# Optimization experiments

Measured on AMD Instinct MI355X. Metric: run time of the kernel, lower is better.

The kernel has to match this reference:

```python
import jax, jax.numpy as jnp
import numpy as np

EPS = 1e-8
TAU = 1.0


def graph_conv(h_in, adj, W, b):
    # h: [N, D_out]
    h = h_in @ W
    nrm = jnp.linalg.norm(h, axis=1, keepdims=True)
    h_norm = h / jnp.maximum(nrm, EPS)  # F.normalize with eps clamp
    # cosine-sim logits + log-adjacency mask -> row softmax
    logits = (h_norm @ h_norm.T) / TAU + jnp.log(adj + EPS)  # [N, N]
    attn = jax.nn.softmax(logits, axis=1)
    return attn @ h + b


def setup_inputs() -> dict:
    key = jax.random.key(0)
    ks = jax.random.split(key, 20)
    N, F, H, C = 4096, 512, 128, 16

    def xavier(k, fan_in, fan_out):
        s = float(np.sqrt(6.0 / (fan_in + fan_out)))
        return jax.random.uniform(k, (fan_in, fan_out), minval=-s, maxval=s, dtype=jnp.float32)

    return {
        "x": jax.random.normal(ks[0], (N, F), dtype=jnp.float32),
        "adj_low": jax.random.uniform(ks[1], (N, N), dtype=jnp.float32),
        "adj_high": jax.random.uniform(ks[2], (N, N), dtype=jnp.float32),
        "adj_mid": jax.random.uniform(ks[3], (N, N), dtype=jnp.float32),
        "w_low0": xavier(ks[4], F, H), "b_low0": jnp.zeros((H,), jnp.float32),
        "w_high0": xavier(ks[5], F, H), "b_high0": jnp.zeros((H,), jnp.float32),
        "w_mid0": xavier(ks[6], F, H), "b_mid0": jnp.zeros((H,), jnp.float32),
        "w_low1": xavier(ks[7], H, C), "b_low1": jnp.zeros((C,), jnp.float32),
        "w_high1": xavier(ks[8], H, C), "b_high1": jnp.zeros((C,), jnp.float32),
        "w_mid1": xavier(ks[9], H, C), "b_mid1": jnp.zeros((C,), jnp.float32),
        "g0": jnp.ones((3,), jnp.float32),
        "g1": jnp.ones((3,), jnp.float32),
    }


def reference(x, adj_low, adj_high, adj_mid,
              w_low0, b_low0, w_high0, b_high0, w_mid0, b_mid0,
              w_low1, b_low1, w_high1, b_high1, w_mid1, b_mid1,
              g0, g1):
    # layer 0 (inner layer: ReLU; dropout p=0 in eval mode -> identity)
    hl = jax.nn.relu(graph_conv(x, adj_low, w_low0, b_low0))
    hh = jax.nn.relu(graph_conv(x, adj_high, w_high0, b_high0))
    hm = jax.nn.relu(graph_conv(x, adj_mid, w_mid0, b_mid0))
    w = jax.nn.softmax(g0)
    h = w[0] * hl + w[1] * hh + w[2] * hm

    # layer 1 (final layer: no activation)
    hl = graph_conv(h, adj_low, w_low1, b_low1)
    hh = graph_conv(h, adj_high, w_high1, b_high1)
    hm = graph_conv(h, adj_mid, w_mid1, b_mid1)
    w = jax.nn.softmax(g1)
    h = w[0] * hl + w[1] * hh + w[2] * hm

    return jax.nn.log_softmax(h, axis=-1)
```

## Files before the change

### kernel.cpp

```cpp
#include <hip/hip_runtime.h>

#define N_NODES 4096
#define F_IN 512
#define H_DIM 128
#define C_DIM 16
#define EPSF 1e-8f
#define LOG2E 1.4426950408889634f
#define SMAX 2.0f
#define NKS0 8
#define KLEN0 (N_NODES / NKS0)
#define NT0 (KLEN0 / 32)
#define NKS1 8

typedef __attribute__((ext_vector_type(8))) short bf16x8;
typedef __attribute__((ext_vector_type(4))) short bf16x4;
typedef __attribute__((ext_vector_type(4))) float f32x4;

__device__ __forceinline__ ushort f2bf(float f){
  union { float f; unsigned u; } v; v.f = f;
  unsigned u = v.u;
  return (ushort)((u + 0x7fffu + ((u >> 16) & 1u)) >> 16);
}
__device__ __forceinline__ float bf2f(ushort h){
  union { unsigned u; float f; } v; v.u = ((unsigned)h) << 16;
  return v.f;
}

__global__ __launch_bounds__(256) void proj0_kernel(
    const float* __restrict__ x,
    const float* __restrict__ Wl, const float* __restrict__ Wh,
    const float* __restrict__ Wm,
    ushort* __restrict__ hn, ushort* __restrict__ hvT)
{
  const int t = threadIdx.x;
  const int d = t & 127;
  const int half = t >> 7;
  const int r0 = blockIdx.x * 8;
  __shared__ float xs[8][F_IN];
  for (int i = t; i < 8 * F_IN; i += 256)
    xs[i >> 9][i & 511] = x[(size_t)(r0 + (i >> 9)) * F_IN + (i & 511)];
  __syncthreads();

  float acc0[8], acc1[8], acc2[8];
#pragma unroll
  for (int r = 0; r < 8; r++) { acc0[r] = 0.f; acc1[r] = 0.f; acc2[r] = 0.f; }

  const int k0 = half * (F_IN / 2);
  for (int k = k0; k < k0 + F_IN / 2; k++) {
    float wl = Wl[k * H_DIM + d];
    float wh = Wh[k * H_DIM + d];
    float wm = Wm[k * H_DIM + d];
#pragma unroll
    for (int r = 0; r < 8; r++) {
      float xv = xs[r][k];
      acc0[r] = fmaf(xv, wl, acc0[r]);
      acc1[r] = fmaf(xv, wh, acc1[r]);
      acc2[r] = fmaf(xv, wm, acc2[r]);
    }
  }

  __shared__ float part[3][8][128];
  if (half == 1) {
#pragma unroll
    for (int r = 0; r < 8; r++) {
      part[0][r][d] = acc0[r]; part[1][r][d] = acc1[r]; part[2][r][d] = acc2[r];
    }
  }
  __syncthreads();
  if (half == 0) {
#pragma unroll
    for (int r = 0; r < 8; r++) {
      acc0[r] += part[0][r][d]; acc1[r] += part[1][r][d]; acc2[r] += part[2][r][d];
    }
  }

  __shared__ float red[24][2];
  const int wv = t >> 6;
  const int lane = t & 63;

#define REDUCE_BRANCH(ACC, B)                                        \
  _Pragma("unroll")                                                  \
  for (int r = 0; r < 8; r++) {                                      \
    float v = ACC[r] * ACC[r];                                       \
    v += __shfl_down(v, 32); v += __shfl_down(v, 16);                \
    v += __shfl_down(v, 8);  v += __shfl_down(v, 4);                 \
    v += __shfl_down(v, 2);  v += __shfl_down(v, 1);                 \
    if (lane == 0) red[(B) * 8 + r][wv] = v;                         \
  }
  if (half == 0) {
    REDUCE_BRANCH(acc0, 0)
    REDUCE_BRANCH(acc1, 1)
    REDUCE_BRANCH(acc2, 2)
  }
  __syncthreads();

#define WRITE_BRANCH(ACC, B)                                                   \
  _Pragma("unroll")                                                            \
  for (int r = 0; r < 8; r++) {                                                \
    float nrm = sqrtf(red[(B) * 8 + r][0] + red[(B) * 8 + r][1]);              \
    float rn = 1.0f / fmaxf(nrm, EPSF);                                        \
    float h = ACC[r];                                                          \
    hn[((size_t)(B) * N_NODES + r0 + r) * H_DIM + d] = f2bf(h * rn);           \
    hvT[((size_t)(B) * H_DIM + d) * N_NODES + r0 + r] = f2bf(h);               \
  }
  if (half == 0) {
    WRITE_BRANCH(acc0, 0)
    WRITE_BRANCH(acc1, 1)
    WRITE_BRANCH(acc2, 2)
  }
#undef REDUCE_BRANCH
#undef WRITE_BRANCH
}

__global__ __launch_bounds__(512) void flash0_kernel(
    const ushort* __restrict__ hn, const ushort* __restrict__ hvT,
    const float* __restrict__ adj_l, const float* __restrict__ adj_h,
    const float* __restrict__ adj_m,
    float* __restrict__ pl0, ushort* __restrict__ pO)
{
  const int tid = threadIdx.x;
  const int w = tid >> 6;
  const int lane = tid & 63;
  const int lr = lane & 15;
  const int lg = lane >> 4;
  const int ks = blockIdx.y;
  const int b = blockIdx.z;
  const int q0 = blockIdx.x * 128 + w * 16;
  const float* adj = (b == 0) ? adj_l : (b == 1) ? adj_h : adj_m;
  const ushort* Qg = hn + (size_t)b * N_NODES * H_DIM;
  const ushort* VTg = hvT + (size_t)b * H_DIM * N_NODES;
  const int kbase = ks * KLEN0;

  __shared__ ushort sK[2][32 * 128];
  __shared__ ushort sV[2][128 * 32];

  bf16x8 qf[4];
  {
    const ushort* qp = Qg + (size_t)(q0 + lr) * H_DIM + lg * 8;
#pragma unroll
    for (int u = 0; u < 4; u++) qf[u] = *(const bf16x8*)(qp + 32 * u);
  }

  f32x4 o[8];
#pragma unroll
  for (int dt = 0; dt < 8; dt++) o[dt] = (f32x4){0.f, 0.f, 0.f, 0.f};
  float lsum = 0.f;

  const float* arow = adj + (size_t)(q0 + lr) * N_NODES + kbase;

  const int kk = tid >> 4, kc = tid & 15;
  const size_t kOff = (size_t)kk * H_DIM + ((size_t)(kc ^ (kk & 7)) << 3);
  const int dV = tid >> 2, vc = tid & 3;
  const size_t vOff = (size_t)dV * N_NODES + ((size_t)(vc ^ ((dV >> 1) & 3)) << 3);

#define STAGE(BUF, K0)                                                         \
  {                                                                            \
    __builtin_amdgcn_global_load_lds(Qg + (size_t)(K0) * H_DIM + kOff,         \
        (char*)&sK[BUF][0] + w * 1024, 16, 0, 0);                              \
    __builtin_amdgcn_global_load_lds(VTg + (K0) + vOff,                        \
        (char*)&sV[BUF][0] + w * 1024, 16, 0, 0);                              \
  }

  f32x4 a0c, a1c, a0n, a1n;
  STAGE(0, kbase)
  a0c = *(const f32x4*)(arow + lg * 4);
  a1c = *(const f32x4*)(arow + 16 + lg * 4);

  for (int t = 0; t < NT0; t++) {
    const int cur = t & 1;
    __builtin_amdgcn_s_barrier();
    __builtin_amdgcn_sched_barrier(0);
    if (t + 1 < NT0) {
      STAGE(cur ^ 1, kbase + (t + 1) * 32)
      a0n = *(const f32x4*)(arow + (t + 1) * 32 + lg * 4);
      a1n = *(const f32x4*)(arow + (t + 1) * 32 + 16 + lg * 4);
    }
    if (t + 1 < NT0) { asm volatile("s_waitcnt vmcnt(4)" ::: "memory"); }
    else             { asm volatile("s_waitcnt vmcnt(0)" ::: "memory"); }
    __builtin_amdgcn_sched_barrier(0);
    __builtin_amdgcn_s_barrier();
    __builtin_amdgcn_sched_barrier(0);

    __builtin_amdgcn_s_setprio(1);
    f32x4 s0 = (f32x4){0.f, 0.f, 0.f, 0.f};
    f32x4 s1 = (f32x4){0.f, 0.f, 0.f, 0.f};
    const char* sKc = (const char*)&sK[cur][0];
#pragma unroll
    for (int u = 0; u < 4; u++) {
      const int c0 = lg + 4 * u;
      bf16x8 kf0 = *(const bf16x8*)(sKc + lr * 256 + ((c0 ^ (lr & 7)) << 4));
      bf16x8 kf1 = *(const bf16x8*)(sKc + (lr + 16) * 256 + ((c0 ^ (lr & 7)) << 4));
      s0 = __builtin_amdgcn_mfma_f32_16x16x32_bf16(kf0, qf[u], s0, 0, 0, 0);
      s1 = __builtin_amdgcn_mfma_f32_16x16x32_bf16(kf1, qf[u], s1, 0, 0, 0);
    }
    bf16x4 pf0, pf1;
#pragma unroll
    for (int r = 0; r < 4; r++) {
      float p0 = exp2f(fmaf(s0[r], LOG2E, -SMAX)) * (a0c[r] + EPSF);
      float p1 = exp2f(fmaf(s1[r], LOG2E, -SMAX)) * (a1c[r] + EPSF);
      lsum += p0 + p1;
      pf0[r] = (short)f2bf(p0);
      pf1[r] = (short)f2bf(p1);
    }
    const char* sVc = (const char*)&sV[cur][0];
#pragma unroll
    for (int dt = 0; dt < 8; dt++) {
      const int dd = dt * 16 + lr;
      const int sw = (dd >> 1) & 3;
      bf16x4 vf0 = *(const bf16x4*)(sVc + dd * 64 +
                     ((((lg >> 1) + 0) ^ sw) << 4) + (lg & 1) * 8);
      bf16x4 vf1 = *(const bf16x4*)(sVc + dd * 64 +
                     ((((lg >> 1) + 2) ^ sw) << 4) + (lg & 1) * 8);
      o[dt] = __builtin_amdgcn_mfma_f32_16x16x16bf16_1k(pf0, vf0, o[dt], 0, 0, 0);
      o[dt] = __builtin_amdgcn_mfma_f32_16x16x16bf16_1k(pf1, vf1, o[dt], 0, 0, 0);
    }
    __builtin_amdgcn_s_setprio(0);
    a0c = a0n; a1c = a1n;
  }
#undef STAGE

  const int ps = b * NKS0 + ks;
  float psum = lsum;
  psum += __shfl_xor(psum, 16);
  psum += __shfl_xor(psum, 32);
  if (lg == 0) pl0[(size_t)ps * N_NODES + q0 + lr] = psum;
#pragma unroll
  for (int dt = 0; dt < 8; dt++) {
#pragma unroll
    for (int r = 0; r < 4; r++) {
      pO[((size_t)ps * N_NODES + q0 + lg * 4 + r) * H_DIM + dt * 16 + lr] =
          f2bf(o[dt][r]);
    }
  }
}

__global__ __launch_bounds__(128) void mix1_kernel(
    const float* __restrict__ pl0, const ushort* __restrict__ pO,
    const float* __restrict__ bl0, const float* __restrict__ bh0,
    const float* __restrict__ bm0,
    const float* __restrict__ Wl1, const float* __restrict__ Wh1,
    const float* __restrict__ Wm1,
    const float* __restrict__ g0,
    ushort* __restrict__ hn1b, ushort* __restrict__ hbT)
{
  const int q = blockIdx.x;
  const int t = threadIdx.x;
  float ga = g0[0], gb = g0[1], gc = g0[2];
  float gm = fmaxf(ga, fmaxf(gb, gc));
  float e0 = expf(ga - gm), e1 = expf(gb - gm), e2 = expf(gc - gm);
  float ei = 1.0f / (e0 + e1 + e2);

  __shared__ float Ls[3];
  if (t < 3) {
    float L = 0.f;
#pragma unroll
    for (int ks = 0; ks < NKS0; ks++) L += pl0[(size_t)(t * NKS0 + ks) * N_NODES + q];
    Ls[t] = L;
  }
  float O0 = 0.f, O1 = 0.f, O2 = 0.f;
#pragma unroll
  for (int ks = 0; ks < NKS0; ks++) {
    O0 += bf2f(pO[((size_t)(0 * NKS0 + ks) * N_NODES + q) * H_DIM + t]);
    O1 += bf2f(pO[((size_t)(1 * NKS0 + ks) * N_NODES + q) * H_DIM + t]);
    O2 += bf2f(pO[((size_t)(2 * NKS0 + ks) * N_NODES + q) * H_DIM + t]);
  }
  __syncthreads();

  __shared__ float hc[H_DIM];
  hc[t] = e0 * ei * fmaxf(O0 / Ls[0] + bl0[t], 0.f)
        + e1 * ei * fmaxf(O1 / Ls[1] + bh0[t], 0.f)
        + e2 * ei * fmaxf(O2 / Ls[2] + bm0[t], 0.f);
  __syncthreads();

  __shared__ float shb[48];
  if (t < 48) {
    const int b = t >> 4, j = t & 15;
    const float* W = (b == 0) ? Wl1 : (b == 1) ? Wh1 : Wm1;
    float s = 0.f;
    for (int k = 0; k < H_DIM; k++) s = fmaf(hc[k], W[k * C_DIM + j], s);
    shb[t] = s;
  }
  __syncthreads();
  __shared__ float rns[3];
  if (t < 3) {
    float s = 0.f;
#pragma unroll
    for (int j = 0; j < C_DIM; j++) { float u = shb[t * C_DIM + j]; s = fmaf(u, u, s); }
    rns[t] = 1.0f / fmaxf(sqrtf(s), EPSF);
  }
  __syncthreads();
  if (t < 48) {
    const int b = t >> 4, j = t & 15;
    hbT[((size_t)b * C_DIM + j) * N_NODES + q] = f2bf(shb[t]);
    hn1b[((size_t)b * N_NODES + q) * C_DIM + j] = f2bf(shb[t] * rns[b]);
  }
}

__global__ __launch_bounds__(256) void flash1_kernel(
    const ushort* __restrict__ hn1b, const ushort* __restrict__ hbT,
    const float* __restrict__ adj_l, const float* __restrict__ adj_h,
    const float* __restrict__ adj_m,
    float* __restrict__ pl, float* __restrict__ pacc)
{
  const int tid = threadIdx.x;
  const int wid = tid >> 6;
  const int lane = tid & 63;
  const int lr = lane & 15;
  const int lg = lane >> 4;
  const int qblk = blockIdx.x * 64;
  const int q0 = qblk + wid * 16;
  const int ks = blockIdx.y;
  const int b = blockIdx.z;
  const float* adj = (b == 0) ? adj_l : (b == 1) ? adj_h : adj_m;
  const ushort* Qn = hn1b + (size_t)b * N_NODES * C_DIM;
  const ushort* VT = hbT + (size_t)b * C_DIM * N_NODES;
  const int kbase = ks * (N_NODES / NKS1);
  const int nt = (N_NODES / NKS1) / 32;

  __shared__ float sAdj[2][64 * 32];

  const bf16x4 qf = *(const bf16x4*)(Qn + (size_t)(q0 + lr) * C_DIM + lg * 4);
  const f32x4 zero = (f32x4){0.f, 0.f, 0.f, 0.f};
  f32x4 o = zero;
  float lsum = 0.f;
  const ushort* vrow = VT + (size_t)lr * N_NODES;

  const int rowA = tid >> 3, cA = tid & 7;
  const int rowB = rowA + 32;
  const size_t aOffA = (size_t)rowA * N_NODES + ((size_t)(cA ^ (rowA & 7)) << 2);
  const size_t aOffB = (size_t)rowB * N_NODES + ((size_t)(cA ^ (rowB & 7)) << 2);
  const float* adjq = adj + (size_t)qblk * N_NODES;

#define STAGE1(BUF, K0)                                                        \
  {                                                                            \
    const float* asrc = adjq + (K0);                                           \
    __builtin_amdgcn_global_load_lds(asrc + aOffA,                             \
        (char*)&sAdj[BUF][0] + wid * 1024, 16, 0, 0);                          \
    __builtin_amdgcn_global_load_lds(asrc + aOffB,                             \
        (char*)&sAdj[BUF][0] + 4096 + wid * 1024, 16, 0, 0);                   \
  }

  STAGE1(0, kbase)

  const int rowL = wid * 16 + lr;
  const int adr0 = rowL * 32 + ((lg ^ (rowL & 7)) << 2);
  const int adr1 = rowL * 32 + (((4 + lg) ^ (rowL & 7)) << 2);

  for (int t = 0; t < nt; t++) {
    const int cur = t & 1;
    __syncthreads();
    if (t + 1 < nt) STAGE1(cur ^ 1, kbase + (t + 1) * 32)

    const int k0 = kbase + t * 32;
    bf16x4 kf0 = *(const bf16x4*)(Qn + (size_t)(k0 + lr) * C_DIM + lg * 4);
    bf16x4 kf1 = *(const bf16x4*)(Qn + (size_t)(k0 + 16 + lr) * C_DIM + lg * 4);
    f32x4 s0 = __builtin_amdgcn_mfma_f32_16x16x16bf16_1k(kf0, qf, zero, 0, 0, 0);
    f32x4 s1 = __builtin_amdgcn_mfma_f32_16x16x16bf16_1k(kf1, qf, zero, 0, 0, 0);
    f32x4 a0 = *(const f32x4*)&sAdj[cur][adr0];
    f32x4 a1 = *(const f32x4*)&sAdj[cur][adr1];
    bf16x4 pf0, pf1;
#pragma unroll
    for (int r = 0; r < 4; r++) {
      float e0 = exp2f(fmaf(s0[r], LOG2E, -SMAX));
      float e1 = exp2f(fmaf(s1[r], LOG2E, -SMAX));
      float p0 = e0 * (a0[r] + EPSF);
      float p1 = e1 * (a1[r] + EPSF);
      lsum += p0 + p1;
      pf0[r] = (short)f2bf(p0);
      pf1[r] = (short)f2bf(p1);
    }
    bf16x4 vf0 = *(const bf16x4*)(vrow + k0 + lg * 4);
    bf16x4 vf1 = *(const bf16x4*)(vrow + k0 + 16 + lg * 4);
    o = __builtin_amdgcn_mfma_f32_16x16x16bf16_1k(pf0, vf0, o, 0, 0, 0);
    o = __builtin_amdgcn_mfma_f32_16x16x16bf16_1k(pf1, vf1, o, 0, 0, 0);
  }
#undef STAGE1

  const int ps = b * NKS1 + ks;
  float psum = lsum;
  psum += __shfl_xor(psum, 16);
  psum += __shfl_xor(psum, 32);
  if (lg == 0) pl[(size_t)ps * N_NODES + q0 + lr] = psum;
#pragma unroll
  for (int r = 0; r < 4; r++)
    pacc[((size_t)ps * N_NODES + q0 + lg * 4 + r) * C_DIM + lr] = o[r];
}

__global__ __launch_bounds__(256) void combine1_kernel(
    const float* __restrict__ pl, const float* __restrict__ pacc,
    float* __restrict__ o1)
{
  const int q = blockIdx.x * 256 + threadIdx.x;
  const int b = blockIdx.y;
  float L = 0.f;
  f32x4 out0 = (f32x4){0,0,0,0}, out1 = (f32x4){0,0,0,0},
        out2 = (f32x4){0,0,0,0}, out3 = (f32x4){0,0,0,0};
#pragma unroll
  for (int ks = 0; ks < NKS1; ks++) {
    const size_t pidx = (size_t)(b * NKS1 + ks) * N_NODES + q;
    L += pl[pidx];
    const f32x4* pa = (const f32x4*)(pacc + pidx * C_DIM);
    out0 += pa[0]; out1 += pa[1]; out2 += pa[2]; out3 += pa[3];
  }
  float invL = 1.0f / L;
  f32x4* dst = (f32x4*)(o1 + ((size_t)b * N_NODES + q) * C_DIM);
  dst[0] = out0 * invL; dst[1] = out1 * invL; dst[2] = out2 * invL; dst[3] = out3 * invL;
}

__global__ __launch_bounds__(256) void final_kernel(
    const float* __restrict__ o1,
    const float* __restrict__ bl1, const float* __restrict__ bh1,
    const float* __restrict__ bm1,
    const float* __restrict__ g1, float* __restrict__ out)
{
  const int q = blockIdx.x * 256 + threadIdx.x;
  float ga = g1[0], gb = g1[1], gc = g1[2];
  float gm = fmaxf(ga, fmaxf(gb, gc));
  float e0 = expf(ga - gm), e1 = expf(gb - gm), e2 = expf(gc - gm);
  float ei = 1.0f / (e0 + e1 + e2);
  float w0 = e0 * ei, w1 = e1 * ei, w2 = e2 * ei;
  const size_t NC = (size_t)N_NODES * C_DIM;

  float v[16];
#pragma unroll
  for (int i = 0; i < 4; i++) {
    f32x4 a = ((const f32x4*)(o1 + (size_t)q * C_DIM))[i];
    f32x4 bA = ((const f32x4*)(o1 + NC + (size_t)q * C_DIM))[i];
    f32x4 c = ((const f32x4*)(o1 + 2 * NC + (size_t)q * C_DIM))[i];
    f32x4 xl = ((const f32x4*)bl1)[i];
    f32x4 xh = ((const f32x4*)bh1)[i];
    f32x4 xm = ((const f32x4*)bm1)[i];
#pragma unroll
    for (int j = 0; j < 4; j++)
      v[i * 4 + j] = w0 * (a[j] + xl[j]) + w1 * (bA[j] + xh[j]) + w2 * (c[j] + xm[j]);
  }
  float mx = -1e30f;
#pragma unroll
  for (int j = 0; j < 16; j++) mx = fmaxf(mx, v[j]);
  float se = 0.f;
#pragma unroll
  for (int j = 0; j < 16; j++) se += expf(v[j] - mx);
  float lse = mx + logf(se);
  f32x4* dst = (f32x4*)(out + (size_t)q * C_DIM);
#pragma unroll
  for (int i = 0; i < 4; i++) {
    f32x4 r;
#pragma unroll
    for (int j = 0; j < 4; j++) r[j] = v[i * 4 + j] - lse;
    dst[i] = r;
  }
}

extern "C" void kernel_launch(void* const* d_in, const int* in_sizes, int n_in,
                              void* d_out, int out_size, void* d_ws, size_t ws_size,
                              hipStream_t stream) {
  (void)in_sizes; (void)n_in; (void)out_size; (void)ws_size;
  const float* x     = (const float*)d_in[0];
  const float* adj_l = (const float*)d_in[1];
  const float* adj_h = (const float*)d_in[2];
  const float* adj_m = (const float*)d_in[3];
  const float* w_l0  = (const float*)d_in[4];
  const float* b_l0  = (const float*)d_in[5];
  const float* w_h0  = (const float*)d_in[6];
  const float* b_h0  = (const float*)d_in[7];
  const float* w_m0  = (const float*)d_in[8];
  const float* b_m0  = (const float*)d_in[9];
  const float* w_l1  = (const float*)d_in[10];
  const float* b_l1  = (const float*)d_in[11];
  const float* w_h1  = (const float*)d_in[12];
  const float* b_h1  = (const float*)d_in[13];
  const float* w_m1  = (const float*)d_in[14];
  const float* b_m1  = (const float*)d_in[15];
  const float* g0    = (const float*)d_in[16];
  const float* g1    = (const float*)d_in[17];
  float* out = (float*)d_out;

  char* ws = (char*)d_ws;
  ushort* hn  = (ushort*)(ws);
  ushort* hvT = (ushort*)(ws + (3u << 20));
  ushort* hn1b= (ushort*)(ws + (6u << 20));
  ushort* hbT = (ushort*)(ws + (6u << 20) + (384u << 10));
  float*  pl0 = (float*)(ws + (12u << 20));
  ushort* pO  = (ushort*)(ws + (12u << 20) + (512u << 10));
  float*  pl  = (float*)(ws + (12u << 20));
  float*  pacc= (float*)(ws + (13u << 20));
  float*  o1  = (float*)(ws + (20u << 20));

  proj0_kernel<<<dim3(512), dim3(256), 0, stream>>>(x, w_l0, w_h0, w_m0, hn, hvT);
  flash0_kernel<<<dim3(32, NKS0, 3), dim3(512), 0, stream>>>(hn, hvT, adj_l, adj_h, adj_m,
                                                             pl0, pO);
  mix1_kernel<<<dim3(4096), dim3(128), 0, stream>>>(pl0, pO, b_l0, b_h0, b_m0,
                                                    w_l1, w_h1, w_m1, g0, hn1b, hbT);
  flash1_kernel<<<dim3(64, NKS1, 3), dim3(256), 0, stream>>>(hn1b, hbT, adj_l, adj_h, adj_m,
                                                             pl, pacc);
  combine1_kernel<<<dim3(16, 3), dim3(256), 0, stream>>>(pl, pacc, o1);
  final_kernel<<<dim3(16), dim3(256), 0, stream>>>(o1, b_l1, b_h1, b_m1, g1, out);
}
```

Measured before the change: 164.0 us.

## Process two query tiles per wave in flash0 to reuse K/V fragments

Flash0 now runs 4 waves per block instead of 8, with each wave handling 32 query rows as two 16-row tiles. Each K and V fragment read from LDS feeds twice as many MFMAs, which cuts LDS read traffic per unit of work. Staging is split into two loads per thread, and the V tile moves to a k-chunk-major layout without the XOR swizzle. The cost is roughly doubled accumulator and Q register use, fewer waves for hiding latency, and possible LDS bank conflicts in the new unswizzled V layout.

After: 183.3 us. +11.8%, slower.

```diff
diff --git a/kernel.cpp b/kernel.cpp
--- a/kernel.cpp
+++ b/kernel.cpp
@@ -112,7 +112,7 @@
 #undef WRITE_BRANCH
 }
 
-__global__ __launch_bounds__(512) void flash0_kernel(
+__global__ __launch_bounds__(256) void flash0_kernel(
     const ushort* __restrict__ hn, const ushort* __restrict__ hvT,
     const float* __restrict__ adj_l, const float* __restrict__ adj_h,
     const float* __restrict__ adj_m,
@@ -125,46 +125,66 @@
   const int lg = lane >> 4;
   const int ks = blockIdx.y;
   const int b = blockIdx.z;
-  const int q0 = blockIdx.x * 128 + w * 16;
+  const int q0 = blockIdx.x * 128 + w * 32;
   const float* adj = (b == 0) ? adj_l : (b == 1) ? adj_h : adj_m;
   const ushort* Qg = hn + (size_t)b * N_NODES * H_DIM;
   const ushort* VTg = hvT + (size_t)b * H_DIM * N_NODES;
   const int kbase = ks * KLEN0;
 
   __shared__ ushort sK[2][32 * 128];
-  __shared__ ushort sV[2][128 * 32];
-
-  bf16x8 qf[4];
+  __shared__ ushort sV[2][4 * 128 * 8];
+
+  bf16x8 qfA[4], qfB[4];
   {
-    const ushort* qp = Qg + (size_t)(q0 + lr) * H_DIM + lg * 8;
-#pragma unroll
-    for (int u = 0; u < 4; u++) qf[u] = *(const bf16x8*)(qp + 32 * u);
-  }
-
-  f32x4 o[8];
-#pragma unroll
-  for (int dt = 0; dt < 8; dt++) o[dt] = (f32x4){0.f, 0.f, 0.f, 0.f};
-  float lsum = 0.f;
-
-  const float* arow = adj + (size_t)(q0 + lr) * N_NODES + kbase;
-
-  const int kk = tid >> 4, kc = tid & 15;
-  const size_t kOff = (size_t)kk * H_DIM + ((size_t)(kc ^ (kk & 7)) << 3);
-  const int dV = tid >> 2, vc = tid & 3;
-  const size_t vOff = (size_t)dV * N_NODES + ((size_t)(vc ^ ((dV >> 1) & 3)) << 3);
+    const ushort* qpA = Qg + (size_t)(q0 + lr) * H_DIM + lg * 8;
+    const ushort* qpB = qpA + 16 * H_DIM;
+#pragma unroll
+    for (int u = 0; u < 4; u++) {
+      qfA[u] = *(const bf16x8*)(qpA + 32 * u);
+      qfB[u] = *(const bf16x8*)(qpB + 32 * u);
+    }
+  }
+
+  f32x4 oA[8], oB[8];
+#pragma unroll
+  for (int dt = 0; dt < 8; dt++) {
+    oA[dt] = (f32x4){0.f, 0.f, 0.f, 0.f};
+    oB[dt] = (f32x4){0.f, 0.f, 0.f, 0.f};
+  }
+  float lsumA = 0.f, lsumB = 0.f;
+
+  const float* arowA = adj + (size_t)(q0 + lr) * N_NODES + kbase;
+  const float* arowB = arowA + 16 * (size_t)N_NODES;
+
+  const int kk1 = tid >> 4,        kc1 = tid & 15;
+  const int kk2 = (tid + 256) >> 4, kc2 = (tid + 256) & 15;
+  const size_t kOff1 = (size_t)kk1 * H_DIM + ((size_t)(kc1 ^ (kk1 & 7)) << 3);
+  const size_t kOff2 = (size_t)kk2 * H_DIM + ((size_t)(kc2 ^ (kk2 & 7)) << 3);
+  const int ko1 = tid >> 7,        dV1 = tid & 127;
+  const int ko2 = (tid + 256) >> 7, dV2 = (tid + 256) & 127;
+  const size_t vOff1 = (size_t)dV1 * N_NODES + ko1 * 8;
+  const size_t vOff2 = (size_t)dV2 * N_NODES + ko2 * 8;
 
 #define STAGE(BUF, K0)                                                         \
   {                                                                            \
-    __builtin_amdgcn_global_load_lds(Qg + (size_t)(K0) * H_DIM + kOff,         \
+    const ushort* ksrc = Qg + (size_t)(K0) * H_DIM;                            \
+    const ushort* vsrc = VTg + (K0);                                           \
+    __builtin_amdgcn_global_load_lds(ksrc + kOff1,                             \
         (char*)&sK[BUF][0] + w * 1024, 16, 0, 0);                              \
-    __builtin_amdgcn_global_load_lds(VTg + (K0) + vOff,                        \
+    __builtin_amdgcn_global_load_lds(ksrc + kOff2,                             \
+        (char*)&sK[BUF][0] + 4096 + w * 1024, 16, 0, 0);                       \
+    __builtin_amdgcn_global_load_lds(vsrc + vOff1,                             \
         (char*)&sV[BUF][0] + w * 1024, 16, 0, 0);                              \
-  }
-
-  f32x4 a0c, a1c, a0n, a1n;
+    __builtin_amdgcn_global_load_lds(vsrc + vOff2,                             \
+        (char*)&sV[BUF][0] + 4096 + w * 1024, 16, 0, 0);                       \
+  }
+
+  f32x4 a0cA, a1cA, a0cB, a1cB, a0nA, a1nA, a0nB, a1nB;
   STAGE(0, kbase)
-  a0c = *(const f32x4*)(arow + lg * 4);
-  a1c = *(const f32x4*)(arow + 16 + lg * 4);
+  a0cA = *(const f32x4*)(arowA + lg * 4);
+  a1cA = *(const f32x4*)(arowA + 16 + lg * 4);
+  a0cB = *(const f32x4*)(arowB + lg * 4);
+  a1cB = *(const f32x4*)(arowB + 16 + lg * 4);
 
   for (int t = 0; t < NT0; t++) {
     const int cur = t & 1;
@@ -172,64 +192,81 @@
     __builtin_amdgcn_sched_barrier(0);
     if (t + 1 < NT0) {
       STAGE(cur ^ 1, kbase + (t + 1) * 32)
-      a0n = *(const f32x4*)(arow + (t + 1) * 32 + lg * 4);
-      a1n = *(const f32x4*)(arow + (t + 1) * 32 + 16 + lg * 4);
-    }
-    if (t + 1 < NT0) { asm volatile("s_waitcnt vmcnt(4)" ::: "memory"); }
+      a0nA = *(const f32x4*)(arowA + (t + 1) * 32 + lg * 4);
+      a1nA = *(const f32x4*)(arowA + (t + 1) * 32 + 16 + lg * 4);
+      a0nB = *(const f32x4*)(arowB + (t + 1) * 32 + lg * 4);
+      a1nB = *(const f32x4*)(arowB + (t + 1) * 32 + 16 + lg * 4);
+    }
+    if (t + 1 < NT0) { asm volatile("s_waitcnt vmcnt(8)" ::: "memory"); }
     else             { asm volatile("s_waitcnt vmcnt(0)" ::: "memory"); }
     __builtin_amdgcn_sched_barrier(0);
     __builtin_amdgcn_s_barrier();
     __builtin_amdgcn_sched_barrier(0);
 
     __builtin_amdgcn_s_setprio(1);
-    f32x4 s0 = (f32x4){0.f, 0.f, 0.f, 0.f};
-    f32x4 s1 = (f32x4){0.f, 0.f, 0.f, 0.f};
+    f32x4 sA0 = (f32x4){0.f, 0.f, 0.f, 0.f};
+    f32x4 sA1 = (f32x4){0.f, 0.f, 0.f, 0.f};
+    f32x4 sB0 = (f32x4){0.f, 0.f, 0.f, 0.f};
+    f32x4 sB1 = (f32x4){0.f, 0.f, 0.f, 0.f};
     const char* sKc = (const char*)&sK[cur][0];
 #pragma unroll
     for (int u = 0; u < 4; u++) {
       const int c0 = lg + 4 * u;
       bf16x8 kf0 = *(const bf16x8*)(sKc + lr * 256 + ((c0 ^ (lr & 7)) << 4));
       bf16x8 kf1 = *(const bf16x8*)(sKc + (lr + 16) * 256 + ((c0 ^ (lr & 7)) << 4));
-      s0 = __builtin_amdgcn_mfma_f32_16x16x32_bf16(kf0, qf[u], s0, 0, 0, 0);
-      s1 = __builtin_amdgcn_mfma_f32_16x16x32_bf16(kf1, qf[u], s1, 0, 0, 0);
-    }
-    bf16x4 pf0, pf1;
+      sA0 = __builtin_amdgcn_mfma_f32_16x16x32_bf16(kf0, qfA[u], sA0, 0, 0, 0);
+      sA1 = __builtin_amdgcn_mfma_f32_16x16x32_bf16(kf1, qfA[u], sA1, 0, 0, 0);
+      sB0 = __builtin_amdgcn_mfma_f32_16x16x32_bf16(kf0, qfB[u], sB0, 0, 0, 0);
+      sB1 = __builtin_amdgcn_mfma_f32_16x16x32_bf16(kf1, qfB[u], sB1, 0, 0, 0);
+    }
+    bf16x4 pf0A, pf1A, pf0B, pf1B;
 #pragma unroll
     for (int r = 0; r < 4; r++) {
-      float p0 = exp2f(fmaf(s0[r], LOG2E, -SMAX)) * (a0c[r] + EPSF);
-      float p1 = exp2f(fmaf(s1[r], LOG2E, -SMAX)) * (a1c[r] + EPSF);
-      lsum += p0 + p1;
-      pf0[r] = (short)f2bf(p0);
-      pf1[r] = (short)f2bf(p1);
+      float p0A = exp2f(fmaf(sA0[r], LOG2E, -SMAX)) * (a0cA[r] + EPSF);
+      float p1A = exp2f(fmaf(sA1[r], LOG2E, -SMAX)) * (a1cA[r] + EPSF);
+      float p0B = exp2f(fmaf(sB0[r], LOG2E, -SMAX)) * (a0cB[r] + EPSF);
+      float p1B = exp2f(fmaf(sB1[r], LOG2E, -SMAX)) * (a1cB[r] + EPSF);
+      lsumA += p0A + p1A;
+      lsumB += p0B + p1B;
+      pf0A[r] = (short)f2bf(p0A);
+      pf1A[r] = (short)f2bf(p1A);
+      pf0B[r] = (short)f2bf(p0B);
+      pf1B[r] = (short)f2bf(p1B);
     }
     const char* sVc = (const char*)&sV[cur][0];
 #pragma unroll
     for (int dt = 0; dt < 8; dt++) {
       const int dd = dt * 16 + lr;
-      const int sw = (dd >> 1) & 3;
-      bf16x4 vf0 = *(const bf16x4*)(sVc + dd * 64 +
-                     ((((lg >> 1) + 0) ^ sw) << 4) + (lg & 1) * 8);
-      bf16x4 vf1 = *(const bf16x4*)(sVc + dd * 64 +
-                     ((((lg >> 1) + 2) ^ sw) << 4) + (lg & 1) * 8);
-      o[dt] = __builtin_amdgcn_mfma_f32_16x16x16bf16_1k(pf0, vf0, o[dt], 0, 0, 0);
-      o[dt] = __builtin_amdgcn_mfma_f32_16x16x16bf16_1k(pf1, vf1, o[dt], 0, 0, 0);
+      bf16x4 vf0 = *(const bf16x4*)(sVc + (lg >> 1) * 2048 + dd * 16 + (lg & 1) * 8);
+      bf16x4 vf1 = *(const bf16x4*)(sVc + ((lg >> 1) + 2) * 2048 + dd * 16 + (lg & 1) * 8);
+      oA[dt] = __builtin_amdgcn_mfma_f32_16x16x16bf16_1k(pf0A, vf0, oA[dt], 0, 0, 0);
+      oA[dt] = __builtin_amdgcn_mfma_f32_16x16x16bf16_1k(pf1A, vf1, oA[dt], 0, 0, 0);
+      oB[dt] = __builtin_amdgcn_mfma_f32_16x16x16bf16_1k(pf0B, vf0, oB[dt], 0, 0, 0);
+      oB[dt] = __builtin_amdgcn_mfma_f32_16x16x16bf16_1k(pf1B, vf1, oB[dt], 0, 0, 0);
     }
     __builtin_amdgcn_s_setprio(0);
-    a0c = a0n; a1c = a1n;
+    a0cA = a0nA; a1cA = a1nA; a0cB = a0nB; a1cB = a1nB;
   }
 #undef STAGE
 
   const int ps = b * NKS0 + ks;
-  float psum = lsum;
-  psum += __shfl_xor(psum, 16);
-  psum += __shfl_xor(psum, 32);
-  if (lg == 0) pl0[(size_t)ps * N_NODES + q0 + lr] = psum;
+  float psA = lsumA, psB = lsumB;
+  psA += __shfl_xor(psA, 16);
+  psA += __shfl_xor(psA, 32);
+  psB += __shfl_xor(psB, 16);
+  psB += __shfl_xor(psB, 32);
+  if (lg == 0) {
+    pl0[(size_t)ps * N_NODES + q0 + lr] = psA;
+    pl0[(size_t)ps * N_NODES + q0 + 16 + lr] = psB;
+  }
 #pragma unroll
   for (int dt = 0; dt < 8; dt++) {
 #pragma unroll
     for (int r = 0; r < 4; r++) {
       pO[((size_t)ps * N_NODES + q0 + lg * 4 + r) * H_DIM + dt * 16 + lr] =
-          f2bf(o[dt][r]);
+          f2bf(oA[dt][r]);
+      pO[((size_t)ps * N_NODES + q0 + 16 + lg * 4 + r) * H_DIM + dt * 16 + lr] =
+          f2bf(oB[dt][r]);
     }
   }
 }
@@ -487,7 +524,7 @@
   float*  o1  = (float*)(ws + (20u << 20));
 
   proj0_kernel<<<dim3(512), dim3(256), 0, stream>>>(x, w_l0, w_h0, w_m0, hn, hvT);
-  flash0_kernel<<<dim3(32, NKS0, 3), dim3(512), 0, stream>>>(hn, hvT, adj_l, adj_h, adj_m,
+  flash0_kernel<<<dim3(32, NKS0, 3), dim3(256), 0, stream>>>(hn, hvT, adj_l, adj_h, adj_m,
                                                              pl0, pO);
   mix1_kernel<<<dim3(4096), dim3(128), 0, stream>>>(pl0, pO, b_l0, b_h0, b_m0,
                                                     w_l1, w_h1, w_m1, g0, hn1b, hbT);
```
